# Kernel tuning notes

Measured on AMD Instinct MI355X. Metric: run time of the kernel, lower is better.

The kernel has to match this reference:

```python
import jax, jax.numpy as jnp
import numpy as np

H = 128
N = 1024


def _layernorm(x, g, b, eps=1e-5):
    m = x.mean(-1, keepdims=True)
    v = x.var(-1, keepdims=True)  # biased variance, matches torch LayerNorm
    return (x - m) / jnp.sqrt(v + eps) * g + b


def setup_inputs() -> dict:
    key = jax.random.key(0)
    ks = jax.random.split(key, 16)
    w = lambda k, shp: (jax.random.normal(k, shp, dtype=jnp.float32) * 0.05)
    return {
        "embeddings": jax.random.normal(ks[0], (N, H), dtype=jnp.float32),
        "trace_feats": jax.random.uniform(ks[1], (N, 5), dtype=jnp.float32),
        # consolidation_network: Linear(2H,H) -> LN -> GELU -> Linear(H,H//2) -> GELU -> Linear(H//2,1) -> Sigmoid
        "cW1": w(ks[2], (2 * H, H)), "cb1": jnp.zeros((H,), jnp.float32),
        "ln_g": jnp.ones((H,), jnp.float32), "ln_b": jnp.zeros((H,), jnp.float32),
        "cW2": w(ks[3], (H, H // 2)), "cb2": jnp.zeros((H // 2,), jnp.float32),
        "cW3": w(ks[4], (H // 2, 1)), "cb3": jnp.zeros((1,), jnp.float32),
        # association_generator: Linear(2H,H) -> ReLU -> Linear(H,H//4) -> ReLU -> Linear(H//4,1) -> Sigmoid
        "aW1": w(ks[5], (2 * H, H)), "ab1": jnp.zeros((H,), jnp.float32),
        "aW2": w(ks[6], (H, H // 4)), "ab2": jnp.zeros((H // 4,), jnp.float32),
        "aW3": w(ks[7], (H // 4, 1)), "ab3": jnp.zeros((1,), jnp.float32),
        # importance_predictor: Linear(H+5,H//2) -> GELU -> Linear(H//2,1) -> Sigmoid
        "iW1": w(ks[8], (H + 5, H // 2)), "ib1": jnp.zeros((H // 2,), jnp.float32),
        "iW2": w(ks[9], (H // 2, 1)), "ib2": jnp.zeros((1,), jnp.float32),
    }


def reference(embeddings, trace_feats,
              cW1, cb1, ln_g, ln_b, cW2, cb2, cW3, cb3,
              aW1, ab1, aW2, ab2, aW3, ab3,
              iW1, ib1, iW2, ib2):
    n = embeddings.shape[0]
    gelu = lambda x: jax.nn.gelu(x, approximate=False)  # torch nn.GELU default (erf)
    # All ordered pairs i < j, batched in one pass (replaces the O(N^2) Python loop).
    ii, jj = jnp.triu_indices(n, k=1)                    # [P], P = N(N-1)/2
    pair = jnp.concatenate([embeddings[ii], embeddings[jj]], axis=-1)  # [P, 2H]
    # consolidation scores
    h = gelu(_layernorm(pair @ cW1 + cb1, ln_g, ln_b))   # [P, H]
    h = gelu(h @ cW2 + cb2)                               # [P, H//2]
    cons = jax.nn.sigmoid(h @ cW3 + cb3)[:, 0]           # [P]
    # association strengths
    a = jax.nn.relu(pair @ aW1 + ab1)                     # [P, H]
    a = jax.nn.relu(a @ aW2 + ab2)                        # [P, H//4]
    assoc = jax.nn.sigmoid(a @ aW3 + ab3)[:, 0]          # [P]
    # future importance per trace
    fin = jnp.concatenate([embeddings, trace_feats], axis=-1)  # [N, H+5]
    imp = jax.nn.sigmoid(gelu(fin @ iW1 + ib1) @ iW2 + ib2)[:, 0]  # [N]
    return jnp.concatenate([cons, assoc, imp])           # [2P + N]
```

## Files before the change

### kernel.cpp

```cpp
#include <hip/hip_runtime.h>

#define N_TR 1024
#define H_DIM 128
#define P_PAIRS 523776
#define TI 8
#define WS_U    0
#define WS_V    131072
#define WS_UA   262144
#define WS_VA   393216
#define WS_SUMU 524288
#define WS_SUMV 526336
#define WS_FRAG_BYTES 2113536u

typedef __attribute__((ext_vector_type(8))) short bf16x8;
typedef __attribute__((ext_vector_type(4))) float f32x4;

__device__ __forceinline__ short f2bfs(float f) {
  unsigned x = __float_as_uint(f);
  unsigned r = x + 0x7fffu + ((x >> 16) & 1u);
  return (short)(r >> 16);
}
__device__ __forceinline__ unsigned pk_bf16(float f0, float f1) {
  unsigned a0 = __float_as_uint(f0) + 0x8000u;
  unsigned a1 = __float_as_uint(f1) + 0x8000u;
  return __builtin_amdgcn_perm(a1, a0, 0x07060302u);
}
__device__ __forceinline__ float geluf(float x) {
  float u = x * x;
  float p = __builtin_fmaf(u, 0.10294324f, 2.30220820f);
  float e = __builtin_amdgcn_exp2f(x * p);
  float r = __builtin_amdgcn_rcpf(e + 1.0f);
  return __builtin_fmaf(-x, r, x);
}
__device__ __forceinline__ float sigmoidf_(float x) {
  float e = __builtin_amdgcn_exp2f(x * -1.4426950408889634f);
  return __builtin_amdgcn_rcpf(1.0f + e);
}
template <int CTRL>
__device__ __forceinline__ float dpp_add(float x) {
  int v = __builtin_amdgcn_update_dpp(0, __float_as_int(x), CTRL, 0xf, 0xf, true);
  return x + __int_as_float(v);
}
__device__ __forceinline__ float red16(float x) {
  x = dpp_add<0xB1>(x);
  x = dpp_add<0x4E>(x);
  x = dpp_add<0x141>(x);
  x = dpp_add<0x140>(x);
  return x;
}

__global__ __launch_bounds__(256) void k_pre(
    const float* __restrict__ emb, const float* __restrict__ tf,
    const float* __restrict__ cW1, const float* __restrict__ cb1,
    const float* __restrict__ aW1, const float* __restrict__ ab1,
    const float* __restrict__ cW2, const float* __restrict__ aW2,
    const float* __restrict__ iW1, const float* __restrict__ ib1,
    const float* __restrict__ iW2, const float* __restrict__ ib2,
    float* __restrict__ ws, unsigned short* __restrict__ frag,
    float* __restrict__ out)
{
  __shared__ __align__(16) float sE[2][128];
  __shared__ float sRed[2][8];
  const int blk = blockIdx.x;
  const int t = threadIdx.x;
  const int lane = t & 63, wave = t >> 6;

  if (blk < 512) {
    const int b = blk;
    { int r = t >> 7, c = t & 127; sE[r][c] = emb[(b * 2 + r) * 128 + c]; }
    __syncthreads();
    const int k = t & 127;
    const bool cons = (t < 128);
    const float* W    = cons ? cW1 : aW1;
    const float* bias = cons ? cb1 : ab1;
    float* outU = ws + (cons ? WS_U : WS_UA);
    float* outV = ws + (cons ? WS_V : WS_VA);
    float accU0 = 0.f, accU1 = 0.f, accV0 = 0.f, accV1 = 0.f;
    for (int c = 0; c < 128; ++c) {
      float wt = W[c * 128 + k];
      float wb = W[(128 + c) * 128 + k];
      float e0 = sE[0][c], e1 = sE[1][c];
      accU0 = __builtin_fmaf(e0, wt, accU0);
      accU1 = __builtin_fmaf(e1, wt, accU1);
      accV0 = __builtin_fmaf(e0, wb, accV0);
      accV1 = __builtin_fmaf(e1, wb, accV1);
    }
    const float bv = bias[k];
    const float vb0 = accV0 + bv, vb1 = accV1 + bv;
    outU[(b * 2 + 0) * 128 + k] = accU0;
    outU[(b * 2 + 1) * 128 + k] = accU1;
    outV[(b * 2 + 0) * 128 + k] = vb0;
    outV[(b * 2 + 1) * 128 + k] = vb1;
    if (t < 128) {
      float vals[8] = {accU0, accU0 * accU0, accU1, accU1 * accU1,
                       vb0, vb0 * vb0, vb1, vb1 * vb1};
      #pragma unroll
      for (int msk = 1; msk <= 32; msk <<= 1)
        #pragma unroll
        for (int v = 0; v < 8; ++v) vals[v] += __shfl_xor(vals[v], msk, 64);
      if ((t & 63) == 0)
        #pragma unroll
        for (int v = 0; v < 8; ++v) sRed[t >> 6][v] = vals[v];
    }
    __syncthreads();
    if (t == 0) {
      const int i0 = b * 2;
      ws[WS_SUMU + i0 * 2 + 0]       = sRed[0][0] + sRed[1][0];
      ws[WS_SUMU + i0 * 2 + 1]       = sRed[0][1] + sRed[1][1];
      ws[WS_SUMU + (i0 + 1) * 2 + 0] = sRed[0][2] + sRed[1][2];
      ws[WS_SUMU + (i0 + 1) * 2 + 1] = sRed[0][3] + sRed[1][3];
      ws[WS_SUMV + i0 * 2 + 0]       = sRed[0][4] + sRed[1][4];
      ws[WS_SUMV + i0 * 2 + 1]       = sRed[0][5] + sRed[1][5];
      ws[WS_SUMV + (i0 + 1) * 2 + 0] = sRed[0][6] + sRed[1][6];
      ws[WS_SUMV + (i0 + 1) * 2 + 1] = sRed[0][7] + sRed[1][7];
    }
  } else if (blk < 560) {
    int u = (blk - 512) * 256 + t;
    if (u < 8192) {
      int j = u & 7, ln = (u >> 3) & 63, ks = (u >> 9) & 3, nt = u >> 11;
      frag[u] = (unsigned short)f2bfs(cW2[(ks * 32 + (ln >> 4) * 8 + j) * 64 + nt * 16 + (ln & 15)]);
    } else {
      int v = u - 8192;
      int j = v & 7, ln = (v >> 3) & 63, ks = (v >> 9) & 3, nt = v >> 11;
      frag[u] = (unsigned short)f2bfs(aW2[(ks * 32 + (ln >> 4) * 8 + j) * 32 + nt * 16 + (ln & 15)]);
    }
  } else {
    const int r = (blk - 560) * 4 + wave;
    float acc = 0.f;
    for (int c = 0; c < 128; ++c)
      acc = __builtin_fmaf(emb[r * 128 + c], iW1[c * 64 + lane], acc);
    #pragma unroll
    for (int c = 0; c < 5; ++c)
      acc = __builtin_fmaf(tf[r * 5 + c], iW1[(128 + c) * 64 + lane], acc);
    float d = geluf(acc + ib1[lane]) * iW2[lane];
    #pragma unroll
    for (int msk = 32; msk; msk >>= 1) d += __shfl_xor(d, msk, 64);
    if (lane == 0) out[2 * P_PAIRS + r] = sigmoidf_(d + ib2[0]);
  }
}

__global__ __launch_bounds__(256, 4) void k_pairs(
    const float* __restrict__ ws, const unsigned short* __restrict__ frag,
    const float* __restrict__ lng, const float* __restrict__ lnb,
    const float* __restrict__ cb2, const float* __restrict__ cW3,
    const float* __restrict__ cb3,
    const float* __restrict__ ab2, const float* __restrict__ aW3,
    const float* __restrict__ ab3,
    float* __restrict__ out)
{
  const int b = blockIdx.x;
  int jt = (int)((sqrtf((float)b + 1.0f) - 1.0f) * 0.5f);
  while (4 * (jt + 1) * (jt + 1) + 4 * (jt + 1) <= b) ++jt;
  while (jt > 0 && 4 * jt * jt + 4 * jt > b) --jt;
  const int i0 = (b - (4 * jt * jt + 4 * jt)) * 8;

  __shared__ __align__(16) unsigned short sFrag[12288];
  __shared__ __align__(16) float sU[TI][128];
  __shared__ __align__(16) float sUa[TI][128];
  __shared__ __align__(16) float sG[128];
  __shared__ __align__(16) float sB[128];
  __shared__ __align__(16) float sD[4][16][TI];
  __shared__ float sSt[TI * 2];
  const int t = threadIdx.x;
  {
    const uint4* src = (const uint4*)frag;
    uint4* dst = (uint4*)sFrag;
    #pragma unroll
    for (int q = 0; q < 6; ++q) dst[t + q * 256] = src[t + q * 256];
  }
  {
    int r = t >> 5, c4 = (t & 31) * 4;
    *(float4*)&sU[r][c4]  = *(const float4*)(ws + WS_U  + (i0 + r) * 128 + c4);
    *(float4*)&sUa[r][c4] = *(const float4*)(ws + WS_UA + (i0 + r) * 128 + c4);
  }
  if (t < 128) { sG[t] = lng[t]; sB[t] = lnb[t]; }
  if (t < TI * 2) sSt[t] = ws[WS_SUMU + i0 * 2 + t];
  __syncthreads();

  const int lane = t & 63;
  const int wave = t >> 6;
  const int m = lane & 15;
  const int g = lane >> 4;
  const int j = jt * 64 + wave * 16 + m;
  const float* Vrow  = ws + WS_V  + j * 128;
  const float* Varow = ws + WS_VA + j * 128;
  const float svj = ws[WS_SUMV + j * 2];
  const float qvj = ws[WS_SUMV + j * 2 + 1];

  float vC[4][8];
  bf16x8 aV[4];
  #pragma unroll
  for (int ks = 0; ks < 4; ++ks) {
    const int off = ks * 32 + g * 8;
    float4 a0 = *(const float4*)(Vrow + off);
    float4 a1 = *(const float4*)(Vrow + off + 4);
    vC[ks][0]=a0.x; vC[ks][1]=a0.y; vC[ks][2]=a0.z; vC[ks][3]=a0.w;
    vC[ks][4]=a1.x; vC[ks][5]=a1.y; vC[ks][6]=a1.z; vC[ks][7]=a1.w;
    int4 p; p.x = pk_bf16(a0.x, a0.y); p.y = pk_bf16(a0.z, a0.w);
    p.z = pk_bf16(a1.x, a1.y); p.w = pk_bf16(a1.z, a1.w);
    aV[ks] = __builtin_bit_cast(bf16x8, p);
  }

  const f32x4 zero = {0.f, 0.f, 0.f, 0.f};
  {
    f32x4 accD = zero;
    #pragma unroll
    for (int ks = 0; ks < 4; ++ks) {
      const int off = ks * 32 + g * 8;
      const float* ur = sU[m & 7];
      float4 b0 = *(const float4*)(ur + off);
      float4 b1 = *(const float4*)(ur + off + 4);
      int4 p; p.x = pk_bf16(b0.x, b0.y); p.y = pk_bf16(b0.z, b0.w);
      p.z = pk_bf16(b1.x, b1.y); p.w = pk_bf16(b1.z, b1.w);
      accD = __builtin_amdgcn_mfma_f32_16x16x32_bf16(
          aV[ks], __builtin_bit_cast(bf16x8, p), accD, 0, 0, 0);
    }
    if (m < TI) {
      #pragma unroll
      for (int r = 0; r < 4; ++r) sD[wave][g * 4 + r][m] = accD[r];
    }
  }
  __syncthreads();

  float cb2v[4], cw3v[4], ab2v[2], aw3v[2];
  #pragma unroll
  for (int nt = 0; nt < 4; ++nt) { cb2v[nt] = cb2[nt * 16 + m]; cw3v[nt] = cW3[nt * 16 + m]; }
  #pragma unroll
  for (int nt = 0; nt < 2; ++nt) { ab2v[nt] = ab2[nt * 16 + m]; aw3v[nt] = aW3[nt * 16 + m]; }
  const float cb3s = cb3[0], ab3s = ab3[0];
  const bf16x8* bfr = (const bf16x8*)sFrag;
  const float inv128 = 0.0078125f;

  for (int it = 0; it < TI; ++it) {
    const int i = i0 + it;
    if (jt * 64 + wave * 16 + 15 <= i) continue;

    const float su = sSt[it * 2], qu = sSt[it * 2 + 1];
    const float dot = sD[wave][m][it];
    const float mean = (su + svj) * inv128;
    const float ex2  = __builtin_fmaf(2.f, dot, qu + qvj) * inv128;
    const float var  = ex2 - mean * mean;
    const float rstd = rsqrtf(var + 1e-5f);

    const float* su_row  = sU[it];
    const float* sua_row = sUa[it];

    int4 pC[4];
    #pragma unroll
    for (int ks = 0; ks < 4; ++ks) {
      const int off = ks * 32 + g * 8;
      float4 u0 = *(const float4*)(su_row + off);
      float4 u1 = *(const float4*)(su_row + off + 4);
      float4 g0 = *(const float4*)(sG + off);
      float4 g1 = *(const float4*)(sG + off + 4);
      float4 b0 = *(const float4*)(sB + off);
      float4 b1 = *(const float4*)(sB + off + 4);
      float us[8] = {u0.x,u0.y,u0.z,u0.w,u1.x,u1.y,u1.z,u1.w};
      float gg[8] = {g0.x,g0.y,g0.z,g0.w,g1.x,g1.y,g1.z,g1.w};
      float bb[8] = {b0.x,b0.y,b0.z,b0.w,b1.x,b1.y,b1.z,b1.w};
      float y[8];
      #pragma unroll
      for (int s = 0; s < 8; ++s) {
        float x = us[s] + vC[ks][s];
        float tq = (x - mean) * rstd;
        y[s] = geluf(__builtin_fmaf(tq, gg[s], bb[s]));
      }
      pC[ks].x = pk_bf16(y[0], y[1]); pC[ks].y = pk_bf16(y[2], y[3]);
      pC[ks].z = pk_bf16(y[4], y[5]); pC[ks].w = pk_bf16(y[6], y[7]);
    }

    int4 pA[4];
    #pragma unroll
    for (int ks = 0; ks < 4; ++ks) {
      const int off = ks * 32 + g * 8;
      float4 u0 = *(const float4*)(sua_row + off);
      float4 u1 = *(const float4*)(sua_row + off + 4);
      float4 v0 = *(const float4*)(Varow + off);
      float4 v1 = *(const float4*)(Varow + off + 4);
      float us[8] = {u0.x,u0.y,u0.z,u0.w,u1.x,u1.y,u1.z,u1.w};
      float vs[8] = {v0.x,v0.y,v0.z,v0.w,v1.x,v1.y,v1.z,v1.w};
      float r[8];
      #pragma unroll
      for (int s = 0; s < 8; ++s) r[s] = fmaxf(us[s] + vs[s], 0.f);
      pA[ks].x = pk_bf16(r[0], r[1]); pA[ks].y = pk_bf16(r[2], r[3]);
      pA[ks].z = pk_bf16(r[4], r[5]); pA[ks].w = pk_bf16(r[6], r[7]);
    }

    f32x4 accC[4] = {zero, zero, zero, zero};
    f32x4 accA[2] = {zero, zero};
    #pragma unroll
    for (int ks = 0; ks < 4; ++ks) {
      bf16x8 aC = __builtin_bit_cast(bf16x8, pC[ks]);
      bf16x8 aA = __builtin_bit_cast(bf16x8, pA[ks]);
      #pragma unroll
      for (int nt = 0; nt < 4; ++nt)
        accC[nt] = __builtin_amdgcn_mfma_f32_16x16x32_bf16(
            aC, bfr[(nt * 4 + ks) * 64 + lane], accC[nt], 0, 0, 0);
      #pragma unroll
      for (int nt = 0; nt < 2; ++nt)
        accA[nt] = __builtin_amdgcn_mfma_f32_16x16x32_bf16(
            aA, bfr[1024 + (nt * 4 + ks) * 64 + lane], accA[nt], 0, 0, 0);
    }

    float sc[4] = {0.f, 0.f, 0.f, 0.f};
    float sa[4] = {0.f, 0.f, 0.f, 0.f};
    #pragma unroll
    for (int nt = 0; nt < 4; ++nt)
      #pragma unroll
      for (int r = 0; r < 4; ++r)
        sc[r] = __builtin_fmaf(geluf(accC[nt][r] + cb2v[nt]), cw3v[nt], sc[r]);
    #pragma unroll
    for (int nt = 0; nt < 2; ++nt)
      #pragma unroll
      for (int r = 0; r < 4; ++r)
        sa[r] = __builtin_fmaf(fmaxf(accA[nt][r] + ab2v[nt], 0.f), aw3v[nt], sa[r]);
    #pragma unroll
    for (int r = 0; r < 4; ++r) { sc[r] = red16(sc[r]); sa[r] = red16(sa[r]); }

    if (m < 4) {
      const int jr = jt * 64 + wave * 16 + g * 4 + m;
      if (jr > i) {
        const int p = i * (2 * N_TR - i - 1) / 2 + (jr - i - 1);
        out[p]           = sigmoidf_(sc[m] + cb3s);
        out[P_PAIRS + p] = sigmoidf_(sa[m] + ab3s);
      }
    }
  }
}

extern "C" void kernel_launch(void* const* d_in, const int* in_sizes, int n_in,
                              void* d_out, int out_size, void* d_ws, size_t ws_size,
                              hipStream_t stream) {
  const float* emb = (const float*)d_in[0];
  const float* tf  = (const float*)d_in[1];
  const float* cW1 = (const float*)d_in[2];
  const float* cb1 = (const float*)d_in[3];
  const float* lng = (const float*)d_in[4];
  const float* lnb = (const float*)d_in[5];
  const float* cW2 = (const float*)d_in[6];
  const float* cb2 = (const float*)d_in[7];
  const float* cW3 = (const float*)d_in[8];
  const float* cb3 = (const float*)d_in[9];
  const float* aW1 = (const float*)d_in[10];
  const float* ab1 = (const float*)d_in[11];
  const float* aW2 = (const float*)d_in[12];
  const float* ab2 = (const float*)d_in[13];
  const float* aW3 = (const float*)d_in[14];
  const float* ab3 = (const float*)d_in[15];
  const float* iW1 = (const float*)d_in[16];
  const float* ib1 = (const float*)d_in[17];
  const float* iW2 = (const float*)d_in[18];
  const float* ib2 = (const float*)d_in[19];

  float* ws = (float*)d_ws;
  unsigned short* frag = (unsigned short*)((char*)d_ws + WS_FRAG_BYTES);
  float* out = (float*)d_out;

  hipLaunchKernelGGL(k_pre, dim3(816), dim3(256), 0, stream,
                     emb, tf, cW1, cb1, aW1, ab1, cW2, aW2,
                     iW1, ib1, iW2, ib2, ws, frag, out);
  hipLaunchKernelGGL(k_pairs, dim3(1088), dim3(256), 0, stream,
                     ws, frag, lng, lnb, cb2, cW3, cb3, ab2, aW3, ab3, out);
}
```

Before: 173.2 us.

## Use persistent blocks with atomic job queue and smaller row tiles in pair kernel

Turns k_pairs into a persistent kernel: 1280 blocks loop, taking job indices from a global atomic counter (reset in k_pre) instead of one block per tile. The row tile shrinks from 8 to 4 rows, giving 2176 finer jobs for better load balance over the triangular pair space, and the launch-bounds occupancy hint rises from 4 to 5. The bf16 weight fragments are loaded into shared memory once per block rather than once per tile. Costs are an atomic plus extra barriers per job, and less reuse of each V row across i rows since tiles are smaller.

New measurement: 194.5 us. 12.3% more time.

```diff
diff --git a/kernel.cpp b/kernel.cpp
--- a/kernel.cpp
+++ b/kernel.cpp
@@ -3,7 +3,8 @@
 #define N_TR 1024
 #define H_DIM 128
 #define P_PAIRS 523776
-#define TI 8
+#define TI 4
+#define N_JOBS 2176
 #define WS_U    0
 #define WS_V    131072
 #define WS_UA   262144
@@ -11,6 +12,7 @@
 #define WS_SUMU 524288
 #define WS_SUMV 526336
 #define WS_FRAG_BYTES 2113536u
+#define WS_CNT_BYTES  2138112u
 
 typedef __attribute__((ext_vector_type(8))) short bf16x8;
 typedef __attribute__((ext_vector_type(4))) float f32x4;
@@ -57,7 +59,7 @@
     const float* __restrict__ iW1, const float* __restrict__ ib1,
     const float* __restrict__ iW2, const float* __restrict__ ib2,
     float* __restrict__ ws, unsigned short* __restrict__ frag,
-    float* __restrict__ out)
+    int* __restrict__ cnt, float* __restrict__ out)
 {
   __shared__ __align__(16) float sE[2][128];
   __shared__ float sRed[2][8];
@@ -115,6 +117,7 @@
       ws[WS_SUMV + (i0 + 1) * 2 + 1] = sRed[0][7] + sRed[1][7];
     }
   } else if (blk < 560) {
+    if (blk == 512 && t == 0) *cnt = 0;
     int u = (blk - 512) * 256 + t;
     if (u < 8192) {
       int j = u & 7, ln = (u >> 3) & 63, ks = (u >> 9) & 3, nt = u >> 11;
@@ -139,8 +142,9 @@
   }
 }
 
-__global__ __launch_bounds__(256, 4) void k_pairs(
+__global__ __launch_bounds__(256, 5) void k_pairs(
     const float* __restrict__ ws, const unsigned short* __restrict__ frag,
+    int* __restrict__ cnt,
     const float* __restrict__ lng, const float* __restrict__ lnb,
     const float* __restrict__ cb2, const float* __restrict__ cW3,
     const float* __restrict__ cb3,
@@ -148,19 +152,13 @@
     const float* __restrict__ ab3,
     float* __restrict__ out)
 {
-  const int b = blockIdx.x;
-  int jt = (int)((sqrtf((float)b + 1.0f) - 1.0f) * 0.5f);
-  while (4 * (jt + 1) * (jt + 1) + 4 * (jt + 1) <= b) ++jt;
-  while (jt > 0 && 4 * jt * jt + 4 * jt > b) --jt;
-  const int i0 = (b - (4 * jt * jt + 4 * jt)) * 8;
-
   __shared__ __align__(16) unsigned short sFrag[12288];
-  __shared__ __align__(16) float sU[TI][128];
+  __shared__ __align__(16) float sU[TI][132];
   __shared__ __align__(16) float sUa[TI][128];
   __shared__ __align__(16) float sG[128];
   __shared__ __align__(16) float sB[128];
   __shared__ __align__(16) float sD[4][16][TI];
-  __shared__ float sSt[TI * 2];
+  __shared__ int sJob;
   const int t = threadIdx.x;
   {
     const uint4* src = (const uint4*)frag;
@@ -168,59 +166,12 @@
     #pragma unroll
     for (int q = 0; q < 6; ++q) dst[t + q * 256] = src[t + q * 256];
   }
-  {
-    int r = t >> 5, c4 = (t & 31) * 4;
-    *(float4*)&sU[r][c4]  = *(const float4*)(ws + WS_U  + (i0 + r) * 128 + c4);
-    *(float4*)&sUa[r][c4] = *(const float4*)(ws + WS_UA + (i0 + r) * 128 + c4);
-  }
   if (t < 128) { sG[t] = lng[t]; sB[t] = lnb[t]; }
-  if (t < TI * 2) sSt[t] = ws[WS_SUMU + i0 * 2 + t];
-  __syncthreads();
 
   const int lane = t & 63;
   const int wave = t >> 6;
   const int m = lane & 15;
   const int g = lane >> 4;
-  const int j = jt * 64 + wave * 16 + m;
-  const float* Vrow  = ws + WS_V  + j * 128;
-  const float* Varow = ws + WS_VA + j * 128;
-  const float svj = ws[WS_SUMV + j * 2];
-  const float qvj = ws[WS_SUMV + j * 2 + 1];
-
-  float vC[4][8];
-  bf16x8 aV[4];
-  #pragma unroll
-  for (int ks = 0; ks < 4; ++ks) {
-    const int off = ks * 32 + g * 8;
-    float4 a0 = *(const float4*)(Vrow + off);
-    float4 a1 = *(const float4*)(Vrow + off + 4);
-    vC[ks][0]=a0.x; vC[ks][1]=a0.y; vC[ks][2]=a0.z; vC[ks][3]=a0.w;
-    vC[ks][4]=a1.x; vC[ks][5]=a1.y; vC[ks][6]=a1.z; vC[ks][7]=a1.w;
-    int4 p; p.x = pk_bf16(a0.x, a0.y); p.y = pk_bf16(a0.z, a0.w);
-    p.z = pk_bf16(a1.x, a1.y); p.w = pk_bf16(a1.z, a1.w);
-    aV[ks] = __builtin_bit_cast(bf16x8, p);
-  }
-
-  const f32x4 zero = {0.f, 0.f, 0.f, 0.f};
-  {
-    f32x4 accD = zero;
-    #pragma unroll
-    for (int ks = 0; ks < 4; ++ks) {
-      const int off = ks * 32 + g * 8;
-      const float* ur = sU[m & 7];
-      float4 b0 = *(const float4*)(ur + off);
-      float4 b1 = *(const float4*)(ur + off + 4);
-      int4 p; p.x = pk_bf16(b0.x, b0.y); p.y = pk_bf16(b0.z, b0.w);
-      p.z = pk_bf16(b1.x, b1.y); p.w = pk_bf16(b1.z, b1.w);
-      accD = __builtin_amdgcn_mfma_f32_16x16x32_bf16(
-          aV[ks], __builtin_bit_cast(bf16x8, p), accD, 0, 0, 0);
-    }
-    if (m < TI) {
-      #pragma unroll
-      for (int r = 0; r < 4; ++r) sD[wave][g * 4 + r][m] = accD[r];
-    }
-  }
-  __syncthreads();
 
   float cb2v[4], cw3v[4], ab2v[2], aw3v[2];
   #pragma unroll
@@ -229,102 +180,167 @@
   for (int nt = 0; nt < 2; ++nt) { ab2v[nt] = ab2[nt * 16 + m]; aw3v[nt] = aW3[nt * 16 + m]; }
   const float cb3s = cb3[0], ab3s = ab3[0];
   const bf16x8* bfr = (const bf16x8*)sFrag;
+  const f32x4 zero = {0.f, 0.f, 0.f, 0.f};
   const float inv128 = 0.0078125f;
 
-  for (int it = 0; it < TI; ++it) {
-    const int i = i0 + it;
-    if (jt * 64 + wave * 16 + 15 <= i) continue;
-
-    const float su = sSt[it * 2], qu = sSt[it * 2 + 1];
-    const float dot = sD[wave][m][it];
-    const float mean = (su + svj) * inv128;
-    const float ex2  = __builtin_fmaf(2.f, dot, qu + qvj) * inv128;
-    const float var  = ex2 - mean * mean;
-    const float rstd = rsqrtf(var + 1e-5f);
-
-    const float* su_row  = sU[it];
-    const float* sua_row = sUa[it];
-
-    int4 pC[4];
+  for (;;) {
+    if (t == 0) sJob = atomicAdd(cnt, 1);
+    __syncthreads();
+    const int b = sJob;
+    if (b >= N_JOBS) break;
+
+    int jt = (int)sqrtf((float)b * 0.125f);
+    if (jt > 15) jt = 15;
+    while (8 * (jt + 1) * (jt + 2) <= b) ++jt;
+    while (jt > 0 && 8 * jt * (jt + 1) > b) --jt;
+    const int i0 = (b - 8 * jt * (jt + 1)) * TI;
+
+    {
+      const int r = wave, c2 = lane * 2;
+      float2 uu = *(const float2*)(ws + WS_U  + (i0 + r) * 128 + c2);
+      float2 ua = *(const float2*)(ws + WS_UA + (i0 + r) * 128 + c2);
+      sU[r][c2] = uu.x;  sU[r][c2 + 1] = uu.y;
+      sUa[r][c2] = ua.x; sUa[r][c2 + 1] = ua.y;
+    }
+    __syncthreads();
+
+    const int j = jt * 64 + wave * 16 + m;
+    const float* Vrow  = ws + WS_V  + j * 128;
+    const float* Varow = ws + WS_VA + j * 128;
+    const float svj = ws[WS_SUMV + j * 2];
+    const float qvj = ws[WS_SUMV + j * 2 + 1];
+
+    float vC[4][8];
+    bf16x8 aV[4];
     #pragma unroll
     for (int ks = 0; ks < 4; ++ks) {
       const int off = ks * 32 + g * 8;
-      float4 u0 = *(const float4*)(su_row + off);
-      float4 u1 = *(const float4*)(su_row + off + 4);
-      float4 g0 = *(const float4*)(sG + off);
-      float4 g1 = *(const float4*)(sG + off + 4);
-      float4 b0 = *(const float4*)(sB + off);
-      float4 b1 = *(const float4*)(sB + off + 4);
-      float us[8] = {u0.x,u0.y,u0.z,u0.w,u1.x,u1.y,u1.z,u1.w};
-      float gg[8] = {g0.x,g0.y,g0.z,g0.w,g1.x,g1.y,g1.z,g1.w};
-      float bb[8] = {b0.x,b0.y,b0.z,b0.w,b1.x,b1.y,b1.z,b1.w};
-      float y[8];
-      #pragma unroll
-      for (int s = 0; s < 8; ++s) {
-        float x = us[s] + vC[ks][s];
-        float tq = (x - mean) * rstd;
-        y[s] = geluf(__builtin_fmaf(tq, gg[s], bb[s]));
-      }
-      pC[ks].x = pk_bf16(y[0], y[1]); pC[ks].y = pk_bf16(y[2], y[3]);
-      pC[ks].z = pk_bf16(y[4], y[5]); pC[ks].w = pk_bf16(y[6], y[7]);
-    }
-
-    int4 pA[4];
-    #pragma unroll
-    for (int ks = 0; ks < 4; ++ks) {
-      const int off = ks * 32 + g * 8;
-      float4 u0 = *(const float4*)(sua_row + off);
-      float4 u1 = *(const float4*)(sua_row + off + 4);
-      float4 v0 = *(const float4*)(Varow + off);
-      float4 v1 = *(const float4*)(Varow + off + 4);
-      float us[8] = {u0.x,u0.y,u0.z,u0.w,u1.x,u1.y,u1.z,u1.w};
-      float vs[8] = {v0.x,v0.y,v0.z,v0.w,v1.x,v1.y,v1.z,v1.w};
-      float r[8];
-      #pragma unroll
-      for (int s = 0; s < 8; ++s) r[s] = fmaxf(us[s] + vs[s], 0.f);
-      pA[ks].x = pk_bf16(r[0], r[1]); pA[ks].y = pk_bf16(r[2], r[3]);
-      pA[ks].z = pk_bf16(r[4], r[5]); pA[ks].w = pk_bf16(r[6], r[7]);
-    }
-
-    f32x4 accC[4] = {zero, zero, zero, zero};
-    f32x4 accA[2] = {zero, zero};
-    #pragma unroll
-    for (int ks = 0; ks < 4; ++ks) {
-      bf16x8 aC = __builtin_bit_cast(bf16x8, pC[ks]);
-      bf16x8 aA = __builtin_bit_cast(bf16x8, pA[ks]);
+      float4 a0 = *(const float4*)(Vrow + off);
+      float4 a1 = *(const float4*)(Vrow + off + 4);
+      vC[ks][0]=a0.x; vC[ks][1]=a0.y; vC[ks][2]=a0.z; vC[ks][3]=a0.w;
+      vC[ks][4]=a1.x; vC[ks][5]=a1.y; vC[ks][6]=a1.z; vC[ks][7]=a1.w;
+      int4 p; p.x = pk_bf16(a0.x, a0.y); p.y = pk_bf16(a0.z, a0.w);
+      p.z = pk_bf16(a1.x, a1.y); p.w = pk_bf16(a1.z, a1.w);
+      aV[ks] = __builtin_bit_cast(bf16x8, p);
+    }
+
+    {
+      f32x4 accD = zero;
+      #pragma unroll
+      for (int ks = 0; ks < 4; ++ks) {
+        const int off = ks * 32 + g * 8;
+        const float* ur = sU[m & (TI - 1)];
+        float4 b0 = *(const float4*)(ur + off);
+        float4 b1 = *(const float4*)(ur + off + 4);
+        int4 p; p.x = pk_bf16(b0.x, b0.y); p.y = pk_bf16(b0.z, b0.w);
+        p.z = pk_bf16(b1.x, b1.y); p.w = pk_bf16(b1.z, b1.w);
+        accD = __builtin_amdgcn_mfma_f32_16x16x32_bf16(
+            aV[ks], __builtin_bit_cast(bf16x8, p), accD, 0, 0, 0);
+      }
+      if (m < TI) {
+        #pragma unroll
+        for (int r = 0; r < 4; ++r) sD[wave][g * 4 + r][m] = accD[r];
+      }
+    }
+    __syncthreads();
+
+    for (int it = 0; it < TI; ++it) {
+      const int i = i0 + it;
+      if (jt * 64 + wave * 16 + 15 <= i) continue;
+
+      const float su = ws[WS_SUMU + i * 2];
+      const float qu = ws[WS_SUMU + i * 2 + 1];
+      const float dot = sD[wave][m][it];
+      const float mean = (su + svj) * inv128;
+      const float ex2  = __builtin_fmaf(2.f, dot, qu + qvj) * inv128;
+      const float var  = ex2 - mean * mean;
+      const float rstd = rsqrtf(var + 1e-5f);
+
+      const float* su_row  = sU[it];
+      const float* sua_row = sUa[it];
+
+      int4 pC[4];
+      #pragma unroll
+      for (int ks = 0; ks < 4; ++ks) {
+        const int off = ks * 32 + g * 8;
+        float4 u0 = *(const float4*)(su_row + off);
+        float4 u1 = *(const float4*)(su_row + off + 4);
+        float4 g0 = *(const float4*)(sG + off);
+        float4 g1 = *(const float4*)(sG + off + 4);
+        float4 b0 = *(const float4*)(sB + off);
+        float4 b1 = *(const float4*)(sB + off + 4);
+        float us[8] = {u0.x,u0.y,u0.z,u0.w,u1.x,u1.y,u1.z,u1.w};
+        float gg[8] = {g0.x,g0.y,g0.z,g0.w,g1.x,g1.y,g1.z,g1.w};
+        float bb[8] = {b0.x,b0.y,b0.z,b0.w,b1.x,b1.y,b1.z,b1.w};
+        float y[8];
+        #pragma unroll
+        for (int s = 0; s < 8; ++s) {
+          float x = us[s] + vC[ks][s];
+          float tq = (x - mean) * rstd;
+          y[s] = geluf(__builtin_fmaf(tq, gg[s], bb[s]));
+        }
+        pC[ks].x = pk_bf16(y[0], y[1]); pC[ks].y = pk_bf16(y[2], y[3]);
+        pC[ks].z = pk_bf16(y[4], y[5]); pC[ks].w = pk_bf16(y[6], y[7]);
+      }
+
+      int4 pA[4];
+      #pragma unroll
+      for (int ks = 0; ks < 4; ++ks) {
+        const int off = ks * 32 + g * 8;
+        float4 u0 = *(const float4*)(sua_row + off);
+        float4 u1 = *(const float4*)(sua_row + off + 4);
+        float4 v0 = *(const float4*)(Varow + off);
+        float4 v1 = *(const float4*)(Varow + off + 4);
+        float us[8] = {u0.x,u0.y,u0.z,u0.w,u1.x,u1.y,u1.z,u1.w};
+        float vs[8] = {v0.x,v0.y,v0.z,v0.w,v1.x,v1.y,v1.z,v1.w};
+        float r[8];
+        #pragma unroll
+        for (int s = 0; s < 8; ++s) r[s] = fmaxf(us[s] + vs[s], 0.f);
+        pA[ks].x = pk_bf16(r[0], r[1]); pA[ks].y = pk_bf16(r[2], r[3]);
+        pA[ks].z = pk_bf16(r[4], r[5]); pA[ks].w = pk_bf16(r[6], r[7]);
+      }
+
+      f32x4 accC[4] = {zero, zero, zero, zero};
+      f32x4 accA[2] = {zero, zero};
+      #pragma unroll
+      for (int ks = 0; ks < 4; ++ks) {
+        bf16x8 aC = __builtin_bit_cast(bf16x8, pC[ks]);
+        bf16x8 aA = __builtin_bit_cast(bf16x8, pA[ks]);
+        #pragma unroll
+        for (int nt = 0; nt < 4; ++nt)
+          accC[nt] = __builtin_amdgcn_mfma_f32_16x16x32_bf16(
+              aC, bfr[(nt * 4 + ks) * 64 + lane], accC[nt], 0, 0, 0);
+        #pragma unroll
+        for (int nt = 0; nt < 2; ++nt)
+          accA[nt] = __builtin_amdgcn_mfma_f32_16x16x32_bf16(
+              aA, bfr[1024 + (nt * 4 + ks) * 64 + lane], accA[nt], 0, 0, 0);
+      }
+
+      float sc[4] = {0.f, 0.f, 0.f, 0.f};
+      float sa[4] = {0.f, 0.f, 0.f, 0.f};
       #pragma unroll
       for (int nt = 0; nt < 4; ++nt)
-        accC[nt] = __builtin_amdgcn_mfma_f32_16x16x32_bf16(
-            aC, bfr[(nt * 4 + ks) * 64 + lane], accC[nt], 0, 0, 0);
+        #pragma unroll
+        for (int r = 0; r < 4; ++r)
+          sc[r] = __builtin_fmaf(geluf(accC[nt][r] + cb2v[nt]), cw3v[nt], sc[r]);
       #pragma unroll
       for (int nt = 0; nt < 2; ++nt)
-        accA[nt] = __builtin_amdgcn_mfma_f32_16x16x32_bf16(
-            aA, bfr[1024 + (nt * 4 + ks) * 64 + lane], accA[nt], 0, 0, 0);
-    }
-
-    float sc[4] = {0.f, 0.f, 0.f, 0.f};
-    float sa[4] = {0.f, 0.f, 0.f, 0.f};
-    #pragma unroll
-    for (int nt = 0; nt < 4; ++nt)
-      #pragma unroll
-      for (int r = 0; r < 4; ++r)
-        sc[r] = __builtin_fmaf(geluf(accC[nt][r] + cb2v[nt]), cw3v[nt], sc[r]);
-    #pragma unroll
-    for (int nt = 0; nt < 2; ++nt)
-      #pragma unroll
-      for (int r = 0; r < 4; ++r)
-        sa[r] = __builtin_fmaf(fmaxf(accA[nt][r] + ab2v[nt], 0.f), aw3v[nt], sa[r]);
-    #pragma unroll
-    for (int r = 0; r < 4; ++r) { sc[r] = red16(sc[r]); sa[r] = red16(sa[r]); }
-
-    if (m < 4) {
-      const int jr = jt * 64 + wave * 16 + g * 4 + m;
-      if (jr > i) {
-        const int p = i * (2 * N_TR - i - 1) / 2 + (jr - i - 1);
-        out[p]           = sigmoidf_(sc[m] + cb3s);
-        out[P_PAIRS + p] = sigmoidf_(sa[m] + ab3s);
-      }
-    }
+        #pragma unroll
+        for (int r = 0; r < 4; ++r)
+          sa[r] = __builtin_fmaf(fmaxf(accA[nt][r] + ab2v[nt], 0.f), aw3v[nt], sa[r]);
+      #pragma unroll
+      for (int r = 0; r < 4; ++r) { sc[r] = red16(sc[r]); sa[r] = red16(sa[r]); }
+
+      if (m < 4) {
+        const int jr = jt * 64 + wave * 16 + g * 4 + m;
+        if (jr > i) {
+          const int p = i * (2 * N_TR - i - 1) / 2 + (jr - i - 1);
+          out[p]           = sigmoidf_(sc[m] + cb3s);
+          out[P_PAIRS + p] = sigmoidf_(sa[m] + ab3s);
+        }
+      }
+    }
+    __syncthreads();
   }
 }
 
@@ -354,11 +370,12 @@
 
   float* ws = (float*)d_ws;
   unsigned short* frag = (unsigned short*)((char*)d_ws + WS_FRAG_BYTES);
+  int* cnt = (int*)((char*)d_ws + WS_CNT_BYTES);
   float* out = (float*)d_out;
 
   hipLaunchKernelGGL(k_pre, dim3(816), dim3(256), 0, stream,
                      emb, tf, cW1, cb1, aW1, ab1, cW2, aW2,
-                     iW1, ib1, iW2, ib2, ws, frag, out);
-  hipLaunchKernelGGL(k_pairs, dim3(1088), dim3(256), 0, stream,
-                     ws, frag, lng, lnb, cb2, cW3, cb3, ab2, aW3, ab3, out);
-}
+                     iW1, ib1, iW2, ib2, ws, frag, cnt, out);
+  hipLaunchKernelGGL(k_pairs, dim3(1280), dim3(256), 0, stream,
+                     ws, frag, cnt, lng, lnb, cb2, cW3, cb3, ab2, aW3, ab3, out);
+}
```

## Use persistent atomic job queue, fp16 association path, and per-lane LayerNorm dot

Applied to the files above, without the earlier changes.

Turns k_pairs into a persistent kernel of 1024 blocks that pull pair tiles from an atomic counter, which is reset in k_pre. Fragment weights are loaded into LDS once per block instead of once per tile. The association branch now keeps its U/V projections and aW2 in fp16 and uses packed fp16 add/max with the f16 MFMA, which cuts workspace traffic and conversion work. The LayerNorm cross term, previously a separate MFMA staged through LDS, is now computed as a per-lane fp32 dot product reduced with shuffles. This adds an atomic and extra barriers per job, and fp16 range could overflow for large activations.

After: 182.1 us. 1.05x slower.

```diff
diff --git a/kernel.cpp b/kernel.cpp
--- a/kernel.cpp
+++ b/kernel.cpp
@@ -4,21 +4,28 @@
 #define H_DIM 128
 #define P_PAIRS 523776
 #define TI 8
+#define N_JOBS 1088
 #define WS_U    0
 #define WS_V    131072
-#define WS_UA   262144
-#define WS_VA   393216
-#define WS_SUMU 524288
-#define WS_SUMV 526336
-#define WS_FRAG_BYTES 2113536u
+#define WS_SUMU 393216
+#define WS_SUMV 395264
+#define WS_UAH  524288
+#define WS_VAH  655360
+#define WS_FRAG_BYTES 1589248u
+#define WS_CNT_BYTES  1613824u
 
 typedef __attribute__((ext_vector_type(8))) short bf16x8;
+typedef __attribute__((ext_vector_type(8))) _Float16 h16x8;
 typedef __attribute__((ext_vector_type(4))) float f32x4;
 
 __device__ __forceinline__ short f2bfs(float f) {
   unsigned x = __float_as_uint(f);
   unsigned r = x + 0x7fffu + ((x >> 16) & 1u);
   return (short)(r >> 16);
+}
+__device__ __forceinline__ unsigned short f2h(float f) {
+  _Float16 h = (_Float16)f;
+  return __builtin_bit_cast(unsigned short, h);
 }
 __device__ __forceinline__ unsigned pk_bf16(float f0, float f1) {
   unsigned a0 = __float_as_uint(f0) + 0x8000u;
@@ -56,8 +63,9 @@
     const float* __restrict__ cW2, const float* __restrict__ aW2,
     const float* __restrict__ iW1, const float* __restrict__ ib1,
     const float* __restrict__ iW2, const float* __restrict__ ib2,
-    float* __restrict__ ws, unsigned short* __restrict__ frag,
-    float* __restrict__ out)
+    float* __restrict__ ws, unsigned short* __restrict__ wsH,
+    unsigned short* __restrict__ frag,
+    int* __restrict__ cnt, float* __restrict__ out)
 {
   __shared__ __align__(16) float sE[2][128];
   __shared__ float sRed[2][8];
@@ -73,8 +81,6 @@
     const bool cons = (t < 128);
     const float* W    = cons ? cW1 : aW1;
     const float* bias = cons ? cb1 : ab1;
-    float* outU = ws + (cons ? WS_U : WS_UA);
-    float* outV = ws + (cons ? WS_V : WS_VA);
     float accU0 = 0.f, accU1 = 0.f, accV0 = 0.f, accV1 = 0.f;
     for (int c = 0; c < 128; ++c) {
       float wt = W[c * 128 + k];
@@ -87,11 +93,11 @@
     }
     const float bv = bias[k];
     const float vb0 = accV0 + bv, vb1 = accV1 + bv;
-    outU[(b * 2 + 0) * 128 + k] = accU0;
-    outU[(b * 2 + 1) * 128 + k] = accU1;
-    outV[(b * 2 + 0) * 128 + k] = vb0;
-    outV[(b * 2 + 1) * 128 + k] = vb1;
-    if (t < 128) {
+    if (cons) {
+      ws[WS_U + (b * 2 + 0) * 128 + k] = accU0;
+      ws[WS_U + (b * 2 + 1) * 128 + k] = accU1;
+      ws[WS_V + (b * 2 + 0) * 128 + k] = vb0;
+      ws[WS_V + (b * 2 + 1) * 128 + k] = vb1;
       float vals[8] = {accU0, accU0 * accU0, accU1, accU1 * accU1,
                        vb0, vb0 * vb0, vb1, vb1 * vb1};
       #pragma unroll
@@ -101,6 +107,11 @@
       if ((t & 63) == 0)
         #pragma unroll
         for (int v = 0; v < 8; ++v) sRed[t >> 6][v] = vals[v];
+    } else {
+      wsH[WS_UAH + (b * 2 + 0) * 128 + k] = f2h(accU0);
+      wsH[WS_UAH + (b * 2 + 1) * 128 + k] = f2h(accU1);
+      wsH[WS_VAH + (b * 2 + 0) * 128 + k] = f2h(vb0);
+      wsH[WS_VAH + (b * 2 + 1) * 128 + k] = f2h(vb1);
     }
     __syncthreads();
     if (t == 0) {
@@ -115,6 +126,7 @@
       ws[WS_SUMV + (i0 + 1) * 2 + 1] = sRed[0][7] + sRed[1][7];
     }
   } else if (blk < 560) {
+    if (blk == 512 && t == 0) *cnt = 0;
     int u = (blk - 512) * 256 + t;
     if (u < 8192) {
       int j = u & 7, ln = (u >> 3) & 63, ks = (u >> 9) & 3, nt = u >> 11;
@@ -122,7 +134,7 @@
     } else {
       int v = u - 8192;
       int j = v & 7, ln = (v >> 3) & 63, ks = (v >> 9) & 3, nt = v >> 11;
-      frag[u] = (unsigned short)f2bfs(aW2[(ks * 32 + (ln >> 4) * 8 + j) * 32 + nt * 16 + (ln & 15)]);
+      frag[u] = f2h(aW2[(ks * 32 + (ln >> 4) * 8 + j) * 32 + nt * 16 + (ln & 15)]);
     }
   } else {
     const int r = (blk - 560) * 4 + wave;
@@ -140,7 +152,9 @@
 }
 
 __global__ __launch_bounds__(256, 4) void k_pairs(
-    const float* __restrict__ ws, const unsigned short* __restrict__ frag,
+    const float* __restrict__ ws, const unsigned short* __restrict__ wsH,
+    const unsigned short* __restrict__ frag,
+    int* __restrict__ cnt,
     const float* __restrict__ lng, const float* __restrict__ lnb,
     const float* __restrict__ cb2, const float* __restrict__ cW3,
     const float* __restrict__ cb3,
@@ -148,19 +162,13 @@
     const float* __restrict__ ab3,
     float* __restrict__ out)
 {
-  const int b = blockIdx.x;
-  int jt = (int)((sqrtf((float)b + 1.0f) - 1.0f) * 0.5f);
-  while (4 * (jt + 1) * (jt + 1) + 4 * (jt + 1) <= b) ++jt;
-  while (jt > 0 && 4 * jt * jt + 4 * jt > b) --jt;
-  const int i0 = (b - (4 * jt * jt + 4 * jt)) * 8;
-
   __shared__ __align__(16) unsigned short sFrag[12288];
   __shared__ __align__(16) float sU[TI][128];
-  __shared__ __align__(16) float sUa[TI][128];
+  __shared__ __align__(16) unsigned short sUaH[TI][128];
   __shared__ __align__(16) float sG[128];
   __shared__ __align__(16) float sB[128];
-  __shared__ __align__(16) float sD[4][16][TI];
   __shared__ float sSt[TI * 2];
+  __shared__ int sJob;
   const int t = threadIdx.x;
   {
     const uint4* src = (const uint4*)frag;
@@ -168,59 +176,12 @@
     #pragma unroll
     for (int q = 0; q < 6; ++q) dst[t + q * 256] = src[t + q * 256];
   }
-  {
-    int r = t >> 5, c4 = (t & 31) * 4;
-    *(float4*)&sU[r][c4]  = *(const float4*)(ws + WS_U  + (i0 + r) * 128 + c4);
-    *(float4*)&sUa[r][c4] = *(const float4*)(ws + WS_UA + (i0 + r) * 128 + c4);
-  }
   if (t < 128) { sG[t] = lng[t]; sB[t] = lnb[t]; }
-  if (t < TI * 2) sSt[t] = ws[WS_SUMU + i0 * 2 + t];
-  __syncthreads();
 
   const int lane = t & 63;
   const int wave = t >> 6;
   const int m = lane & 15;
   const int g = lane >> 4;
-  const int j = jt * 64 + wave * 16 + m;
-  const float* Vrow  = ws + WS_V  + j * 128;
-  const float* Varow = ws + WS_VA + j * 128;
-  const float svj = ws[WS_SUMV + j * 2];
-  const float qvj = ws[WS_SUMV + j * 2 + 1];
-
-  float vC[4][8];
-  bf16x8 aV[4];
-  #pragma unroll
-  for (int ks = 0; ks < 4; ++ks) {
-    const int off = ks * 32 + g * 8;
-    float4 a0 = *(const float4*)(Vrow + off);
-    float4 a1 = *(const float4*)(Vrow + off + 4);
-    vC[ks][0]=a0.x; vC[ks][1]=a0.y; vC[ks][2]=a0.z; vC[ks][3]=a0.w;
-    vC[ks][4]=a1.x; vC[ks][5]=a1.y; vC[ks][6]=a1.z; vC[ks][7]=a1.w;
-    int4 p; p.x = pk_bf16(a0.x, a0.y); p.y = pk_bf16(a0.z, a0.w);
-    p.z = pk_bf16(a1.x, a1.y); p.w = pk_bf16(a1.z, a1.w);
-    aV[ks] = __builtin_bit_cast(bf16x8, p);
-  }
-
-  const f32x4 zero = {0.f, 0.f, 0.f, 0.f};
-  {
-    f32x4 accD = zero;
-    #pragma unroll
-    for (int ks = 0; ks < 4; ++ks) {
-      const int off = ks * 32 + g * 8;
-      const float* ur = sU[m & 7];
-      float4 b0 = *(const float4*)(ur + off);
-      float4 b1 = *(const float4*)(ur + off + 4);
-      int4 p; p.x = pk_bf16(b0.x, b0.y); p.y = pk_bf16(b0.z, b0.w);
-      p.z = pk_bf16(b1.x, b1.y); p.w = pk_bf16(b1.z, b1.w);
-      accD = __builtin_amdgcn_mfma_f32_16x16x32_bf16(
-          aV[ks], __builtin_bit_cast(bf16x8, p), accD, 0, 0, 0);
-    }
-    if (m < TI) {
-      #pragma unroll
-      for (int r = 0; r < 4; ++r) sD[wave][g * 4 + r][m] = accD[r];
-    }
-  }
-  __syncthreads();
 
   float cb2v[4], cw3v[4], ab2v[2], aw3v[2];
   #pragma unroll
@@ -228,103 +189,145 @@
   #pragma unroll
   for (int nt = 0; nt < 2; ++nt) { ab2v[nt] = ab2[nt * 16 + m]; aw3v[nt] = aW3[nt * 16 + m]; }
   const float cb3s = cb3[0], ab3s = ab3[0];
-  const bf16x8* bfr = (const bf16x8*)sFrag;
+  const bf16x8* bfr  = (const bf16x8*)sFrag;
+  const h16x8*  bfrA = (const h16x8*)sFrag + 1024;
+  const f32x4 zero = {0.f, 0.f, 0.f, 0.f};
+  const h16x8 hzero = {0, 0, 0, 0, 0, 0, 0, 0};
   const float inv128 = 0.0078125f;
 
-  for (int it = 0; it < TI; ++it) {
-    const int i = i0 + it;
-    if (jt * 64 + wave * 16 + 15 <= i) continue;
-
-    const float su = sSt[it * 2], qu = sSt[it * 2 + 1];
-    const float dot = sD[wave][m][it];
-    const float mean = (su + svj) * inv128;
-    const float ex2  = __builtin_fmaf(2.f, dot, qu + qvj) * inv128;
-    const float var  = ex2 - mean * mean;
-    const float rstd = rsqrtf(var + 1e-5f);
-
-    const float* su_row  = sU[it];
-    const float* sua_row = sUa[it];
-
-    int4 pC[4];
+  for (;;) {
+    if (t == 0) sJob = atomicAdd(cnt, 1);
+    __syncthreads();
+    const int b = sJob;
+    if (b >= N_JOBS) break;
+
+    int jt = (int)((sqrtf((float)b + 1.0f) - 1.0f) * 0.5f);
+    while (4 * (jt + 1) * (jt + 1) + 4 * (jt + 1) <= b) ++jt;
+    while (jt > 0 && 4 * jt * jt + 4 * jt > b) --jt;
+    const int i0 = (b - (4 * jt * jt + 4 * jt)) * TI;
+
+    {
+      int r = t >> 5, c4 = (t & 31) * 4;
+      *(float4*)&sU[r][c4] = *(const float4*)(ws + WS_U + (i0 + r) * 128 + c4);
+      *(ushort4*)&sUaH[r][c4] = *(const ushort4*)(wsH + WS_UAH + (i0 + r) * 128 + c4);
+    }
+    if (t < TI * 2) sSt[t] = ws[WS_SUMU + i0 * 2 + t];
+    __syncthreads();
+
+    const int j = jt * 64 + wave * 16 + m;
+    const float* Vrow = ws + WS_V + j * 128;
+    const float svj = ws[WS_SUMV + j * 2];
+    const float qvj = ws[WS_SUMV + j * 2 + 1];
+
+    float vC[4][8];
+    h16x8 vAh[4];
     #pragma unroll
     for (int ks = 0; ks < 4; ++ks) {
       const int off = ks * 32 + g * 8;
-      float4 u0 = *(const float4*)(su_row + off);
-      float4 u1 = *(const float4*)(su_row + off + 4);
-      float4 g0 = *(const float4*)(sG + off);
-      float4 g1 = *(const float4*)(sG + off + 4);
-      float4 b0 = *(const float4*)(sB + off);
-      float4 b1 = *(const float4*)(sB + off + 4);
-      float us[8] = {u0.x,u0.y,u0.z,u0.w,u1.x,u1.y,u1.z,u1.w};
-      float gg[8] = {g0.x,g0.y,g0.z,g0.w,g1.x,g1.y,g1.z,g1.w};
-      float bb[8] = {b0.x,b0.y,b0.z,b0.w,b1.x,b1.y,b1.z,b1.w};
-      float y[8];
-      #pragma unroll
-      for (int s = 0; s < 8; ++s) {
-        float x = us[s] + vC[ks][s];
-        float tq = (x - mean) * rstd;
-        y[s] = geluf(__builtin_fmaf(tq, gg[s], bb[s]));
-      }
-      pC[ks].x = pk_bf16(y[0], y[1]); pC[ks].y = pk_bf16(y[2], y[3]);
-      pC[ks].z = pk_bf16(y[4], y[5]); pC[ks].w = pk_bf16(y[6], y[7]);
-    }
-
-    int4 pA[4];
-    #pragma unroll
-    for (int ks = 0; ks < 4; ++ks) {
-      const int off = ks * 32 + g * 8;
-      float4 u0 = *(const float4*)(sua_row + off);
-      float4 u1 = *(const float4*)(sua_row + off + 4);
-      float4 v0 = *(const float4*)(Varow + off);
-      float4 v1 = *(const float4*)(Varow + off + 4);
-      float us[8] = {u0.x,u0.y,u0.z,u0.w,u1.x,u1.y,u1.z,u1.w};
-      float vs[8] = {v0.x,v0.y,v0.z,v0.w,v1.x,v1.y,v1.z,v1.w};
-      float r[8];
-      #pragma unroll
-      for (int s = 0; s < 8; ++s) r[s] = fmaxf(us[s] + vs[s], 0.f);
-      pA[ks].x = pk_bf16(r[0], r[1]); pA[ks].y = pk_bf16(r[2], r[3]);
-      pA[ks].z = pk_bf16(r[4], r[5]); pA[ks].w = pk_bf16(r[6], r[7]);
-    }
-
-    f32x4 accC[4] = {zero, zero, zero, zero};
-    f32x4 accA[2] = {zero, zero};
-    #pragma unroll
-    for (int ks = 0; ks < 4; ++ks) {
-      bf16x8 aC = __builtin_bit_cast(bf16x8, pC[ks]);
-      bf16x8 aA = __builtin_bit_cast(bf16x8, pA[ks]);
+      float4 a0 = *(const float4*)(Vrow + off);
+      float4 a1 = *(const float4*)(Vrow + off + 4);
+      vC[ks][0]=a0.x; vC[ks][1]=a0.y; vC[ks][2]=a0.z; vC[ks][3]=a0.w;
+      vC[ks][4]=a1.x; vC[ks][5]=a1.y; vC[ks][6]=a1.z; vC[ks][7]=a1.w;
+      vAh[ks] = *(const h16x8*)(wsH + WS_VAH + j * 128 + off);
+    }
+
+    for (int it = 0; it < TI; ++it) {
+      const int i = i0 + it;
+      if (jt * 64 + wave * 16 + 15 <= i) continue;
+
+      const float* su_row = sU[it];
+
+      float xc[4][8];
+      float d = 0.f;
+      #pragma unroll
+      for (int ks = 0; ks < 4; ++ks) {
+        const int off = ks * 32 + g * 8;
+        float4 u0 = *(const float4*)(su_row + off);
+        float4 u1 = *(const float4*)(su_row + off + 4);
+        float us[8] = {u0.x,u0.y,u0.z,u0.w,u1.x,u1.y,u1.z,u1.w};
+        #pragma unroll
+        for (int s = 0; s < 8; ++s) {
+          xc[ks][s] = us[s] + vC[ks][s];
+          d = __builtin_fmaf(us[s], vC[ks][s], d);
+        }
+      }
+      d += __shfl_xor(d, 16, 64);
+      d += __shfl_xor(d, 32, 64);
+
+      h16x8 pA[4];
+      #pragma unroll
+      for (int ks = 0; ks < 4; ++ks) {
+        const int off = ks * 32 + g * 8;
+        h16x8 ua = *(const h16x8*)&sUaH[it][off];
+        pA[ks] = __builtin_elementwise_max(ua + vAh[ks], hzero);
+      }
+
+      const float su = sSt[it * 2], qu = sSt[it * 2 + 1];
+      const float mean = (su + svj) * inv128;
+      const float ex2  = __builtin_fmaf(2.f, d, qu + qvj) * inv128;
+      const float var  = ex2 - mean * mean;
+      const float rstd = rsqrtf(var + 1e-5f);
+
+      int4 pC[4];
+      #pragma unroll
+      for (int ks = 0; ks < 4; ++ks) {
+        const int off = ks * 32 + g * 8;
+        float4 g0 = *(const float4*)(sG + off);
+        float4 g1 = *(const float4*)(sG + off + 4);
+        float4 b0 = *(const float4*)(sB + off);
+        float4 b1 = *(const float4*)(sB + off + 4);
+        float gg[8] = {g0.x,g0.y,g0.z,g0.w,g1.x,g1.y,g1.z,g1.w};
+        float bb[8] = {b0.x,b0.y,b0.z,b0.w,b1.x,b1.y,b1.z,b1.w};
+        float y[8];
+        #pragma unroll
+        for (int s = 0; s < 8; ++s) {
+          float tq = (xc[ks][s] - mean) * rstd;
+          y[s] = geluf(__builtin_fmaf(tq, gg[s], bb[s]));
+        }
+        pC[ks].x = pk_bf16(y[0], y[1]); pC[ks].y = pk_bf16(y[2], y[3]);
+        pC[ks].z = pk_bf16(y[4], y[5]); pC[ks].w = pk_bf16(y[6], y[7]);
+      }
+
+      f32x4 accC[4] = {zero, zero, zero, zero};
+      f32x4 accA[2] = {zero, zero};
+      #pragma unroll
+      for (int ks = 0; ks < 4; ++ks) {
+        bf16x8 aC = __builtin_bit_cast(bf16x8, pC[ks]);
+        #pragma unroll
+        for (int nt = 0; nt < 4; ++nt)
+          accC[nt] = __builtin_amdgcn_mfma_f32_16x16x32_bf16(
+              aC, bfr[(nt * 4 + ks) * 64 + lane], accC[nt], 0, 0, 0);
+        #pragma unroll
+        for (int nt = 0; nt < 2; ++nt)
+          accA[nt] = __builtin_amdgcn_mfma_f32_16x16x32_f16(
+              pA[ks], bfrA[(nt * 4 + ks) * 64 + lane], accA[nt], 0, 0, 0);
+      }
+
+      float sc[4] = {0.f, 0.f, 0.f, 0.f};
+      float sa[4] = {0.f, 0.f, 0.f, 0.f};
       #pragma unroll
       for (int nt = 0; nt < 4; ++nt)
-        accC[nt] = __builtin_amdgcn_mfma_f32_16x16x32_bf16(
-            aC, bfr[(nt * 4 + ks) * 64 + lane], accC[nt], 0, 0, 0);
+        #pragma unroll
+        for (int r = 0; r < 4; ++r)
+          sc[r] = __builtin_fmaf(geluf(accC[nt][r] + cb2v[nt]), cw3v[nt], sc[r]);
       #pragma unroll
       for (int nt = 0; nt < 2; ++nt)
-        accA[nt] = __builtin_amdgcn_mfma_f32_16x16x32_bf16(
-            aA, bfr[1024 + (nt * 4 + ks) * 64 + lane], accA[nt], 0, 0, 0);
-    }
-
-    float sc[4] = {0.f, 0.f, 0.f, 0.f};
-    float sa[4] = {0.f, 0.f, 0.f, 0.f};
-    #pragma unroll
-    for (int nt = 0; nt < 4; ++nt)
-      #pragma unroll
-      for (int r = 0; r < 4; ++r)
-        sc[r] = __builtin_fmaf(geluf(accC[nt][r] + cb2v[nt]), cw3v[nt], sc[r]);
-    #pragma unroll
-    for (int nt = 0; nt < 2; ++nt)
-      #pragma unroll
-      for (int r = 0; r < 4; ++r)
-        sa[r] = __builtin_fmaf(fmaxf(accA[nt][r] + ab2v[nt], 0.f), aw3v[nt], sa[r]);
-    #pragma unroll
-    for (int r = 0; r < 4; ++r) { sc[r] = red16(sc[r]); sa[r] = red16(sa[r]); }
-
-    if (m < 4) {
-      const int jr = jt * 64 + wave * 16 + g * 4 + m;
-      if (jr > i) {
-        const int p = i * (2 * N_TR - i - 1) / 2 + (jr - i - 1);
-        out[p]           = sigmoidf_(sc[m] + cb3s);
-        out[P_PAIRS + p] = sigmoidf_(sa[m] + ab3s);
-      }
-    }
+        #pragma unroll
+        for (int r = 0; r < 4; ++r)
+          sa[r] = __builtin_fmaf(fmaxf(accA[nt][r] + ab2v[nt], 0.f), aw3v[nt], sa[r]);
+      #pragma unroll
+      for (int r = 0; r < 4; ++r) { sc[r] = red16(sc[r]); sa[r] = red16(sa[r]); }
+
+      if (m < 4) {
+        const int jr = jt * 64 + wave * 16 + g * 4 + m;
+        if (jr > i) {
+          const int p = i * (2 * N_TR - i - 1) / 2 + (jr - i - 1);
+          out[p]           = sigmoidf_(sc[m] + cb3s);
+          out[P_PAIRS + p] = sigmoidf_(sa[m] + ab3s);
+        }
+      }
+    }
+    __syncthreads();
   }
 }
 
@@ -353,12 +356,14 @@
   const float* ib2 = (const float*)d_in[19];
 
   float* ws = (float*)d_ws;
+  unsigned short* wsH = (unsigned short*)d_ws;
   unsigned short* frag = (unsigned short*)((char*)d_ws + WS_FRAG_BYTES);
+  int* cnt = (int*)((char*)d_ws + WS_CNT_BYTES);
   float* out = (float*)d_out;
 
   hipLaunchKernelGGL(k_pre, dim3(816), dim3(256), 0, stream,
                      emb, tf, cW1, cb1, aW1, ab1, cW2, aW2,
-                     iW1, ib1, iW2, ib2, ws, frag, out);
-  hipLaunchKernelGGL(k_pairs, dim3(1088), dim3(256), 0, stream,
-                     ws, frag, lng, lnb, cb2, cW3, cb3, ab2, aW3, ab3, out);
-}
+                     iW1, ib1, iW2, ib2, ws, wsH, frag, cnt, out);
+  hipLaunchKernelGGL(k_pairs, dim3(1024), dim3(256), 0, stream,
+                     ws, wsH, frag, cnt, lng, lnb, cb2, cW3, cb3, ab2, aW3, ab3, out);
+}
```
